# Kernel tuning notes

Hardware: AMD Instinct MI355X
Metric: run time of the kernel (lower is better)

## Reference

```python
import jax, jax.numpy as jnp
import numpy as np

NEG_SLOPE = 0.2  # PyG GATConv default leaky_relu slope


def segment_softmax(logits, seg, num_segments):
    # logits: [E, H], seg: [E] destination node ids
    m = jax.ops.segment_max(logits, seg, num_segments=num_segments)
    m = jnp.where(jnp.isfinite(m), m, 0.0)  # empty segments
    e = jnp.exp(logits - m[seg])
    s = jax.ops.segment_sum(e, seg, num_segments=num_segments)
    return e / (s[seg] + 1e-16)


def gat_conv(x, src, dst, W, att_src, att_dst, bias, heads, out_ch, concat, num_nodes):
    # x: [N, F_in], W: [F_in, heads*out_ch], att_*: [heads, out_ch]
    h = (x @ W).reshape(num_nodes, heads, out_ch)            # [N, H, C]
    a_src = jnp.sum(h * att_src, axis=-1)                    # [N, H]
    a_dst = jnp.sum(h * att_dst, axis=-1)                    # [N, H]
    logits = jax.nn.leaky_relu(a_src[src] + a_dst[dst], NEG_SLOPE)  # [E, H]
    alpha = segment_softmax(logits, dst, num_nodes)          # [E, H]
    msg = h[src] * alpha[..., None]                          # [E, H, C]
    out = jax.ops.segment_sum(msg, dst, num_segments=num_nodes)  # [N, H, C]
    out = out.reshape(num_nodes, heads * out_ch) if concat else out.mean(axis=1)
    return out + bias


def setup_inputs() -> dict:
    key = jax.random.key(0)
    ks = jax.random.split(key, 12)
    N, E = 50000, 800000
    F_in, Hd, H, F_out = 256, 128, 2, 64

    def glorot(k, shape):
        fan = shape[0] + shape[-1]
        return jax.random.normal(k, shape, dtype=jnp.float32) * jnp.sqrt(2.0 / fan)

    x = jax.random.normal(ks[0], (N, F_in), dtype=jnp.float32)
    edge_index = jax.random.randint(ks[1], (2, E), 0, N, dtype=jnp.int32)
    return {
        "x": x,
        "edge_index": edge_index,
        "W1": glorot(ks[2], (F_in, H * Hd)),
        "att_src1": glorot(ks[3], (H, Hd)),
        "att_dst1": glorot(ks[4], (H, Hd)),
        "b1": jnp.zeros((H * Hd,), dtype=jnp.float32),
        "W2": glorot(ks[5], (H * Hd, F_out)),
        "att_src2": glorot(ks[6], (1, F_out)),
        "att_dst2": glorot(ks[7], (1, F_out)),
        "b2": jnp.zeros((F_out,), dtype=jnp.float32),
    }


def reference(x, edge_index, W1, att_src1, att_dst1, b1, W2, att_src2, att_dst2, b2):
    N = x.shape[0]
    # PyG GATConv default: add self loops
    ar = jnp.arange(N, dtype=edge_index.dtype)
    src = jnp.concatenate([edge_index[0], ar])
    dst = jnp.concatenate([edge_index[1], ar])
    # dropout layers are identity in eval mode
    h = gat_conv(x, src, dst, W1, att_src1, att_dst1, b1,
                 heads=2, out_ch=128, concat=True, num_nodes=N)
    h = jax.nn.elu(h)
    out = gat_conv(h, src, dst, W2, att_src2, att_dst2, b2,
                   heads=1, out_ch=64, concat=False, num_nodes=N)
    return jax.nn.log_softmax(out, axis=1)
```

## Files before the change

kernel.cpp:

```cpp
#include <hip/hip_runtime.h>
#include <hip/hip_bf16.h>

typedef unsigned short u16;
typedef short bf8_t __attribute__((ext_vector_type(8)));
typedef float f32x4 __attribute__((ext_vector_type(4)));

__device__ inline u16 f2bf(float f) {
  unsigned u = __float_as_uint(f);
  u += 0x7FFFu + ((u >> 16) & 1u);
  return (u16)(u >> 16);
}
__device__ inline float bf2f(u16 h) { return __uint_as_float(((unsigned)h) << 16); }
__device__ inline float bflo(unsigned u) { return __uint_as_float(u << 16); }
__device__ inline float bfhi(unsigned u) { return __uint_as_float(u & 0xffff0000u); }

__global__ void prep_kernel(const int* __restrict__ ei, int E, int N,
                            int* __restrict__ counts,
                            const float* __restrict__ W1, const float* __restrict__ W2,
                            u16* __restrict__ W1T, u16* __restrict__ W2T, int nbc) {
  if ((int)blockIdx.x < nbc) {
    int e = blockIdx.x * 256 + threadIdx.x;
    int Et = E + N;
    if (e < Et) {
      int d = (e < E) ? ei[E + e] : (e - E);
      atomicAdd(&counts[d], 1);
    }
  } else {
    int idx = (blockIdx.x - nbc) * 256 + threadIdx.x;
    if (idx < 256 * 256) {
      int m = idx >> 8, k = idx & 255;
      W1T[idx] = f2bf(W1[k * 256 + m]);
    } else if (idx < 256 * 256 + 64 * 256) {
      int i = idx - 256 * 256;
      int m = i >> 8, k = i & 255;
      W2T[i] = f2bf(W2[k * 64 + m]);
    }
  }
}

__global__ void block_scan_kernel(const int* __restrict__ counts, int* __restrict__ offsets,
                                  int* __restrict__ bsums, int N) {
  __shared__ int sm[256];
  int tid = threadIdx.x;
  int gid = blockIdx.x * 256 + tid;
  int v = (gid < N) ? counts[gid] : 0;
  int val = v;
  sm[tid] = val;
  __syncthreads();
  for (int off = 1; off < 256; off <<= 1) {
    int o = (tid >= off) ? sm[tid - off] : 0;
    __syncthreads();
    val += o;
    sm[tid] = val;
    __syncthreads();
  }
  if (gid < N) offsets[gid] = val - v;
  if (tid == 255) bsums[blockIdx.x] = val;
}

__global__ void scan_sums_kernel(int* __restrict__ bsums, int* __restrict__ offsets,
                                 int nb, int N) {
  __shared__ int sm[1024];
  int tid = threadIdx.x;
  int v = (tid < nb) ? bsums[tid] : 0;
  int val = v;
  sm[tid] = val;
  __syncthreads();
  for (int off = 1; off < 1024; off <<= 1) {
    int o = (tid >= off) ? sm[tid - off] : 0;
    __syncthreads();
    val += o;
    sm[tid] = val;
    __syncthreads();
  }
  if (tid < nb) bsums[tid] = val - v;
  if (tid == 1023) offsets[N] = val;
}

__global__ void add_base_kernel(int* __restrict__ offsets, int* __restrict__ cursor,
                                const int* __restrict__ bsums, int N) {
  int gid = blockIdx.x * 256 + threadIdx.x;
  if (gid >= N) return;
  int o = offsets[gid] + bsums[blockIdx.x];
  offsets[gid] = o;
  cursor[gid] = o;
}

__global__ void scatter_kernel(const int* __restrict__ ei, int E, int N,
                               int* __restrict__ cursor, int* __restrict__ csr_src) {
  int e = blockIdx.x * blockDim.x + threadIdx.x;
  int Et = E + N;
  if (e >= Et) return;
  int s, d;
  if (e < E) { s = ei[e]; d = ei[E + e]; }
  else       { s = d = e - E; }
  int pos = atomicAdd(&cursor[d], 1);
  csr_src[pos] = s;
}

template<int BM, int BN, int BK, int WM, int WN, bool AF32, int EPI>
__global__ __launch_bounds__(256) void mfma_gemm(const void* __restrict__ Ap,
                                                 const u16* __restrict__ Bt,
                                                 u16* __restrict__ C,
                                                 const float* __restrict__ att_s,
                                                 const float* __restrict__ att_d,
                                                 float* __restrict__ a_s,
                                                 float* __restrict__ a_d,
                                                 int N, int K) {
  constexpr int PAD = 8;
  __shared__ u16 As[BM][BK + PAD];
  __shared__ u16 Bs[BN][BK + PAD];
  const int tid = threadIdx.x;
  const int row0 = blockIdx.x * BM;
  const int w = tid >> 6, lane = tid & 63;
  const int wr = (w / (BN / WN)) * WM;
  const int wc = (w % (BN / WN)) * WN;
  constexpr int MF = WM / 16, NF = WN / 16;
  constexpr int CPR = BK / 8;
  f32x4 acc[MF][NF] = {};

  for (int k0 = 0; k0 < K; k0 += BK) {
    constexpr int ACH = BM * CPR;
#pragma unroll
    for (int c = 0; c < ACH; c += 256) {
      int cc = c + tid;
      int r = cc / CPR, kc = cc % CPR;
      int row = row0 + r;
      if (AF32) {
        const float* A = (const float*)Ap;
        float4 v0 = make_float4(0.f, 0.f, 0.f, 0.f), v1 = v0;
        if (row < N) {
          const float* p = A + (size_t)row * K + k0 + kc * 8;
          v0 = *(const float4*)p;
          v1 = *(const float4*)(p + 4);
        }
        union { __hip_bfloat162 h[4]; uint4 u; } cv;
        cv.h[0] = __float22bfloat162_rn(make_float2(v0.x, v0.y));
        cv.h[1] = __float22bfloat162_rn(make_float2(v0.z, v0.w));
        cv.h[2] = __float22bfloat162_rn(make_float2(v1.x, v1.y));
        cv.h[3] = __float22bfloat162_rn(make_float2(v1.z, v1.w));
        *(uint4*)&As[r][kc * 8] = cv.u;
      } else {
        const u16* A = (const u16*)Ap;
        uint4 v = make_uint4(0, 0, 0, 0);
        if (row < N) v = *(const uint4*)(A + (size_t)row * K + k0 + kc * 8);
        *(uint4*)&As[r][kc * 8] = v;
      }
    }
    constexpr int BCH = BN * CPR;
#pragma unroll
    for (int c = 0; c < BCH; c += 256) {
      int cc = c + tid;
      int r = cc / CPR, kc = cc % CPR;
      *(uint4*)&Bs[r][kc * 8] = *(const uint4*)(Bt + (size_t)r * K + k0 + kc * 8);
    }
    __syncthreads();
    const int lr = lane & 15, lk = (lane >> 4) * 8;
    bf8_t a[MF], b[NF];
#pragma unroll
    for (int mi = 0; mi < MF; ++mi) a[mi] = *(bf8_t*)&As[wr + mi * 16 + lr][lk];
#pragma unroll
    for (int ni = 0; ni < NF; ++ni) b[ni] = *(bf8_t*)&Bs[wc + ni * 16 + lr][lk];
#pragma unroll
    for (int mi = 0; mi < MF; ++mi)
#pragma unroll
      for (int ni = 0; ni < NF; ++ni)
        acc[mi][ni] = __builtin_amdgcn_mfma_f32_16x16x32_bf16(a[mi], b[ni], acc[mi][ni], 0, 0, 0);
    __syncthreads();
  }
#pragma unroll
  for (int mi = 0; mi < MF; ++mi)
#pragma unroll
    for (int ni = 0; ni < NF; ++ni)
#pragma unroll
      for (int r = 0; r < 4; ++r) {
        int row = row0 + wr + mi * 16 + (lane >> 4) * 4 + r;
        int col = wc + ni * 16 + (lane & 15);
        if (row < N) C[(size_t)row * BN + col] = f2bf(acc[mi][ni][r]);
      }

  if (EPI == 1) {
    __shared__ float sm_s[4][64];
    __shared__ float sm_d[4][64];
    float asl[NF], adl[NF];
#pragma unroll
    for (int ni = 0; ni < NF; ++ni) {
      asl[ni] = att_s[wc + ni * 16 + (lane & 15)];
      adl[ni] = att_d[wc + ni * 16 + (lane & 15)];
    }
#pragma unroll
    for (int mi = 0; mi < MF; ++mi)
#pragma unroll
      for (int r = 0; r < 4; ++r) {
        float ps = 0.f, pd = 0.f;
#pragma unroll
        for (int ni = 0; ni < NF; ++ni) {
          float c = acc[mi][ni][r];
          ps += c * asl[ni];
          pd += c * adl[ni];
        }
#pragma unroll
        for (int o = 1; o < 16; o <<= 1) {
          ps += __shfl_xor(ps, o);
          pd += __shfl_xor(pd, o);
        }
        if ((lane & 15) == 0) {
          int row = mi * 16 + (lane >> 4) * 4 + r;
          sm_s[w][row] = ps;
          sm_d[w][row] = pd;
        }
      }
    __syncthreads();
    if (tid < 128) {
      int row = tid & 63, head = tid >> 6;
      int grow = row0 + row;
      if (grow < N) {
        a_s[grow * 2 + head] = sm_s[head * 2 + 0][row] + sm_s[head * 2 + 1][row];
        a_d[grow * 2 + head] = sm_d[head * 2 + 0][row] + sm_d[head * 2 + 1][row];
      }
    }
  } else if (EPI == 2) {
    float asl[NF], adl[NF];
#pragma unroll
    for (int ni = 0; ni < NF; ++ni) {
      asl[ni] = att_s[ni * 16 + (lane & 15)];
      adl[ni] = att_d[ni * 16 + (lane & 15)];
    }
#pragma unroll
    for (int mi = 0; mi < MF; ++mi)
#pragma unroll
      for (int r = 0; r < 4; ++r) {
        float ps = 0.f, pd = 0.f;
#pragma unroll
        for (int ni = 0; ni < NF; ++ni) {
          float c = acc[mi][ni][r];
          ps += c * asl[ni];
          pd += c * adl[ni];
        }
#pragma unroll
        for (int o = 1; o < 16; o <<= 1) {
          ps += __shfl_xor(ps, o);
          pd += __shfl_xor(pd, o);
        }
        int row = row0 + wr + mi * 16 + (lane >> 4) * 4 + r;
        if ((lane & 15) == 0 && row < N) {
          a_s[row] = ps;
          a_d[row] = pd;
        }
      }
  }
}

__global__ void agg1_kernel(const u16* __restrict__ H1, const int* __restrict__ offsets,
                            const int* __restrict__ csr_src,
                            const float* __restrict__ a_src, const float* __restrict__ a_dst,
                            const float* __restrict__ b1, u16* __restrict__ out, int N) {
  __shared__ int4 meta[4][64];
  int wv = threadIdx.x >> 6;
  int lane = threadIdx.x & 63;
  int node = blockIdx.x * 4 + wv;
  if (node >= N) return;
  int off = offsets[node];
  int deg = offsets[node + 1] - off;
  float ad0 = a_dst[node * 2 + 0];
  float ad1 = a_dst[node * 2 + 1];
  bool hi = lane >= 32;
  const char* H1c = (const char*)H1;
  const unsigned loff = (unsigned)(lane * 8);
  float4 acc = make_float4(0.f, 0.f, 0.f, 0.f);
  float den = 0.f;
  const int4* mw = meta[wv];

  auto proc = [&](int4 m) {
    float w = hi ? __int_as_float(m.z) : __int_as_float(m.y);
    uint2 u = *(const uint2*)(H1c + (((unsigned)m.x << 9) + loff));
    den += w;
    acc.x += w * bflo(u.x);
    acc.y += w * bfhi(u.x);
    acc.z += w * bflo(u.y);
    acc.w += w * bfhi(u.y);
  };

  for (int base = 0; base < deg; base += 64) {
    int i = base + lane;
    if (i < deg) {
      int s = csr_src[off + i];
      float l0 = a_src[s * 2 + 0] + ad0;
      float l1 = a_src[s * 2 + 1] + ad1;
      l0 = l0 > 0.f ? l0 : 0.2f * l0;
      l1 = l1 > 0.f ? l1 : 0.2f * l1;
      meta[wv][lane] = make_int4(s, __float_as_int(__expf(l0)), __float_as_int(__expf(l1)), 0);
    }
    int cnt = min(64, deg - base);
    int j = 0;
    for (; j + 4 <= cnt; j += 4) {
      int4 m0 = mw[j], m1 = mw[j + 1], m2 = mw[j + 2], m3 = mw[j + 3];
      proc(m0); proc(m1); proc(m2); proc(m3);
    }
    for (; j < cnt; ++j) proc(mw[j]);
  }
  float inv = 1.f / (den + 1e-16f);
  float4 bb = *(const float4*)(b1 + lane * 4);
  float o0 = acc.x * inv + bb.x;
  float o1 = acc.y * inv + bb.y;
  float o2 = acc.z * inv + bb.z;
  float o3 = acc.w * inv + bb.w;
  o0 = o0 > 0.f ? o0 : expm1f(o0);
  o1 = o1 > 0.f ? o1 : expm1f(o1);
  o2 = o2 > 0.f ? o2 : expm1f(o2);
  o3 = o3 > 0.f ? o3 : expm1f(o3);
  uint2 ov;
  ov.x = (unsigned)f2bf(o0) | ((unsigned)f2bf(o1) << 16);
  ov.y = (unsigned)f2bf(o2) | ((unsigned)f2bf(o3) << 16);
  *(uint2*)(out + (size_t)node * 256 + lane * 4) = ov;
}

__global__ void agg2_kernel(const u16* __restrict__ H2, const int* __restrict__ offsets,
                            const int* __restrict__ csr_src,
                            const float* __restrict__ a_src, const float* __restrict__ a_dst,
                            const float* __restrict__ b2, float* __restrict__ out, int N) {
  __shared__ int2 meta[4][64];
  int wv = threadIdx.x >> 6;
  int lane = threadIdx.x & 63;
  int node = blockIdx.x * 4 + wv;
  if (node >= N) return;
  int off = offsets[node];
  int deg = offsets[node + 1] - off;
  float ad = a_dst[node];
  const int grp = lane >> 3;
  const int l3 = lane & 7;
  const char* H2c = (const char*)H2;
  const unsigned loff = (unsigned)(l3 * 16);
  float acc[8] = {0.f, 0.f, 0.f, 0.f, 0.f, 0.f, 0.f, 0.f};
  float den = 0.f;
  const int2* mw = meta[wv];

  auto proc = [&](int jj) {
    int2 m = mw[jj];
    float w = __int_as_float(m.y);
    uint4 u = *(const uint4*)(H2c + (((unsigned)m.x << 7) + loff));
    den += w;
    acc[0] += w * bflo(u.x); acc[1] += w * bfhi(u.x);
    acc[2] += w * bflo(u.y); acc[3] += w * bfhi(u.y);
    acc[4] += w * bflo(u.z); acc[5] += w * bfhi(u.z);
    acc[6] += w * bflo(u.w); acc[7] += w * bfhi(u.w);
  };

  for (int base = 0; base < deg; base += 64) {
    int i = base + lane;
    if (i < deg) {
      int s = csr_src[off + i];
      float l = a_src[s] + ad;
      l = l > 0.f ? l : 0.2f * l;
      meta[wv][lane] = make_int2(s, __float_as_int(__expf(l)));
    }
    int cnt = min(64, deg - base);
    int j = 0;
    for (; j + 16 <= cnt; j += 16) { proc(j + grp); proc(j + 8 + grp); }
    for (; j + 8 <= cnt; j += 8) proc(j + grp);
    int r = cnt - j;
    if (r > 0 && grp < r) proc(j + grp);
  }
#pragma unroll
  for (int k = 0; k < 8; ++k) {
    acc[k] += __shfl_xor(acc[k], 8);
    acc[k] += __shfl_xor(acc[k], 16);
    acc[k] += __shfl_xor(acc[k], 32);
  }
  den += __shfl_xor(den, 8);
  den += __shfl_xor(den, 16);
  den += __shfl_xor(den, 32);

  float inv = 1.f / (den + 1e-16f);
  float4 b01 = *(const float4*)(b2 + l3 * 8);
  float4 b23 = *(const float4*)(b2 + l3 * 8 + 4);
  float bb[8] = {b01.x, b01.y, b01.z, b01.w, b23.x, b23.y, b23.z, b23.w};
  float v[8];
#pragma unroll
  for (int k = 0; k < 8; ++k) v[k] = acc[k] * inv + bb[k];
  float m = v[0];
#pragma unroll
  for (int k = 1; k < 8; ++k) m = fmaxf(m, v[k]);
  m = fmaxf(m, __shfl_xor(m, 1));
  m = fmaxf(m, __shfl_xor(m, 2));
  m = fmaxf(m, __shfl_xor(m, 4));
  float sum = 0.f;
#pragma unroll
  for (int k = 0; k < 8; ++k) sum += __expf(v[k] - m);
  sum += __shfl_xor(sum, 1);
  sum += __shfl_xor(sum, 2);
  sum += __shfl_xor(sum, 4);
  float ls = m + logf(sum);
  if (lane < 8) {
    float4 o0 = make_float4(v[0] - ls, v[1] - ls, v[2] - ls, v[3] - ls);
    float4 o1 = make_float4(v[4] - ls, v[5] - ls, v[6] - ls, v[7] - ls);
    *(float4*)(out + (size_t)node * 64 + l3 * 8) = o0;
    *(float4*)(out + (size_t)node * 64 + l3 * 8 + 4) = o1;
  }
}

extern "C" void kernel_launch(void* const* d_in, const int* in_sizes, int n_in,
                              void* d_out, int out_size, void* d_ws, size_t ws_size,
                              hipStream_t stream) {
  const float* x   = (const float*)d_in[0];
  const int*   ei  = (const int*)d_in[1];
  const float* W1  = (const float*)d_in[2];
  const float* as1 = (const float*)d_in[3];
  const float* ad1 = (const float*)d_in[4];
  const float* b1  = (const float*)d_in[5];
  const float* W2  = (const float*)d_in[6];
  const float* as2 = (const float*)d_in[7];
  const float* ad2 = (const float*)d_in[8];
  const float* b2  = (const float*)d_in[9];
  float* out = (float*)d_out;

  const int N  = in_sizes[0] / 256;
  const int E  = in_sizes[1] / 2;
  const int Et = E + N;
  const int nb  = (N + 255) / 256;
  const int nbc = (Et + 255) / 256;
  const int nbt = (256 * 256 + 64 * 256 + 255) / 256;

  char* p = (char*)d_ws;
  auto alloc = [&](size_t bytes) -> char* {
    char* r = p;
    p += (bytes + 255) & ~(size_t)255;
    return r;
  };
  u16* H1b     = (u16*)alloc((size_t)N * 256 * 2);
  u16* h1act   = (u16*)alloc((size_t)N * 256 * 2);
  u16* H2b     = (u16*)alloc((size_t)N * 64 * 2);
  u16* W1T     = (u16*)alloc((size_t)256 * 256 * 2);
  u16* W2T     = (u16*)alloc((size_t)64 * 256 * 2);
  float* a_src1 = (float*)alloc((size_t)N * 2 * 4);
  float* a_dst1 = (float*)alloc((size_t)N * 2 * 4);
  float* a_src2 = (float*)alloc((size_t)N * 4);
  float* a_dst2 = (float*)alloc((size_t)N * 4);
  int* counts   = (int*)alloc((size_t)N * 4);
  int* offsets  = (int*)alloc((size_t)(N + 1) * 4);
  int* cursor   = (int*)alloc((size_t)N * 4);
  int* bsums    = (int*)alloc((size_t)1024 * 4);
  int* csr_src  = (int*)alloc((size_t)Et * 4);

  const int tb = 256;

  hipMemsetAsync(counts, 0, (size_t)N * 4, stream);
  prep_kernel<<<nbc + nbt, tb, 0, stream>>>(ei, E, N, counts, W1, W2, W1T, W2T, nbc);
  block_scan_kernel<<<nb, tb, 0, stream>>>(counts, offsets, bsums, N);
  scan_sums_kernel<<<1, 1024, 0, stream>>>(bsums, offsets, nb, N);
  add_base_kernel<<<nb, tb, 0, stream>>>(offsets, cursor, bsums, N);
  scatter_kernel<<<(Et + tb - 1) / tb, tb, 0, stream>>>(ei, E, N, cursor, csr_src);

  mfma_gemm<64, 256, 32, 64, 64, true, 1><<<(N + 63) / 64, tb, 0, stream>>>(
      x, W1T, H1b, as1, ad1, a_src1, a_dst1, N, 256);
  agg1_kernel<<<(N + 3) / 4, tb, 0, stream>>>(H1b, offsets, csr_src, a_src1, a_dst1, b1,
                                              h1act, N);

  mfma_gemm<128, 64, 32, 32, 64, false, 2><<<(N + 127) / 128, tb, 0, stream>>>(
      h1act, W2T, H2b, as2, ad2, a_src2, a_dst2, N, 256);
  agg2_kernel<<<(N + 3) / 4, tb, 0, stream>>>(H2b, offsets, csr_src, a_src2, a_dst2, b2,
                                              out, N);
}
```

Before: 236.2 us.

## Partition count and scatter atomics into 8 destination-range teams

The edge counting and CSR scatter kernels now launch 2048 blocks split into 8 teams, with blockIdx & 7 picking the team. Each team walks every edge but only does atomics for destinations in its own eighth of the node range. Since consecutive blocks belong to different teams, the intent appears to be keeping each team's atomic targets local (for example within one XCD's L2 on MI355X, if blocks are dealt round-robin across XCDs) and cutting cross-die atomic traffic. The cost is that every edge index is read eight times, and correctness depends on no other assumption.

```diff
diff --git a/kernel.cpp b/kernel.cpp
--- a/kernel.cpp
+++ b/kernel.cpp
@@ -14,19 +14,22 @@
 __device__ inline float bflo(unsigned u) { return __uint_as_float(u << 16); }
 __device__ inline float bfhi(unsigned u) { return __uint_as_float(u & 0xffff0000u); }
 
-__global__ void prep_kernel(const int* __restrict__ ei, int E, int N,
+__global__ void prep_kernel(const int* __restrict__ ei, int E, int N, int N8,
                             int* __restrict__ counts,
                             const float* __restrict__ W1, const float* __restrict__ W2,
-                            u16* __restrict__ W1T, u16* __restrict__ W2T, int nbc) {
-  if ((int)blockIdx.x < nbc) {
-    int e = blockIdx.x * 256 + threadIdx.x;
-    int Et = E + N;
-    if (e < Et) {
+                            u16* __restrict__ W1T, u16* __restrict__ W2T, int teamBlocks) {
+  if ((int)blockIdx.x < teamBlocks) {
+    const int team = blockIdx.x & 7;
+    const int tslot = blockIdx.x >> 3;
+    const int TB = teamBlocks >> 3;
+    const int lo = team * N8, hi = min(N, lo + N8);
+    const int Et = E + N;
+    for (int e = tslot * 256 + (int)threadIdx.x; e < Et; e += TB * 256) {
       int d = (e < E) ? ei[E + e] : (e - E);
-      atomicAdd(&counts[d], 1);
+      if (d >= lo && d < hi) atomicAdd(&counts[d], 1);
     }
   } else {
-    int idx = (blockIdx.x - nbc) * 256 + threadIdx.x;
+    int idx = ((int)blockIdx.x - teamBlocks) * 256 + (int)threadIdx.x;
     if (idx < 256 * 256) {
       int m = idx >> 8, k = idx & 255;
       W1T[idx] = f2bf(W1[k * 256 + m]);
@@ -86,16 +89,22 @@
   cursor[gid] = o;
 }
 
-__global__ void scatter_kernel(const int* __restrict__ ei, int E, int N,
-                               int* __restrict__ cursor, int* __restrict__ csr_src) {
-  int e = blockIdx.x * blockDim.x + threadIdx.x;
-  int Et = E + N;
-  if (e >= Et) return;
-  int s, d;
-  if (e < E) { s = ei[e]; d = ei[E + e]; }
-  else       { s = d = e - E; }
-  int pos = atomicAdd(&cursor[d], 1);
-  csr_src[pos] = s;
+__global__ void scatter_kernel(const int* __restrict__ ei, int E, int N, int N8,
+                               int* __restrict__ cursor, int* __restrict__ csr_src,
+                               int teamBlocks) {
+  const int team = blockIdx.x & 7;
+  const int tslot = blockIdx.x >> 3;
+  const int TB = teamBlocks >> 3;
+  const int lo = team * N8, hi = min(N, lo + N8);
+  const int Et = E + N;
+  for (int e = tslot * 256 + (int)threadIdx.x; e < Et; e += TB * 256) {
+    int d = (e < E) ? ei[E + e] : (e - E);
+    if (d >= lo && d < hi) {
+      int s = (e < E) ? ei[e] : d;
+      int pos = atomicAdd(&cursor[d], 1);
+      csr_src[pos] = s;
+    }
+  }
 }
 
 template<int BM, int BN, int BK, int WM, int WN, bool AF32, int EPI>
@@ -417,9 +426,10 @@
   const int N  = in_sizes[0] / 256;
   const int E  = in_sizes[1] / 2;
   const int Et = E + N;
+  const int N8 = (N + 7) / 8;
   const int nb  = (N + 255) / 256;
-  const int nbc = (Et + 255) / 256;
   const int nbt = (256 * 256 + 64 * 256 + 255) / 256;
+  const int teamBlocks = 2048;
 
   char* p = (char*)d_ws;
   auto alloc = [&](size_t bytes) -> char* {
@@ -445,11 +455,12 @@
   const int tb = 256;
 
   hipMemsetAsync(counts, 0, (size_t)N * 4, stream);
-  prep_kernel<<<nbc + nbt, tb, 0, stream>>>(ei, E, N, counts, W1, W2, W1T, W2T, nbc);
+  prep_kernel<<<teamBlocks + nbt, tb, 0, stream>>>(ei, E, N, N8, counts, W1, W2, W1T, W2T,
+                                                   teamBlocks);
   block_scan_kernel<<<nb, tb, 0, stream>>>(counts, offsets, bsums, N);
   scan_sums_kernel<<<1, 1024, 0, stream>>>(bsums, offsets, nb, N);
   add_base_kernel<<<nb, tb, 0, stream>>>(offsets, cursor, bsums, N);
-  scatter_kernel<<<(Et + tb - 1) / tb, tb, 0, stream>>>(ei, E, N, cursor, csr_src);
+  scatter_kernel<<<teamBlocks, tb, 0, stream>>>(ei, E, N, N8, cursor, csr_src, teamBlocks);
 
   mfma_gemm<64, 256, 32, 64, 64, true, 1><<<(N + 63) / 64, tb, 0, stream>>>(
       x, W1T, H1b, as1, ad1, a_src1, a_dst1, N, 256);
```

Result: faster. 223.6 us (-5.4%).
